# Kernel optimization log

Measured on AMD Instinct MI355X. Metric: run time of the kernel, lower is better.

Reference implementation:

```python
import jax, jax.numpy as jnp
import numpy as np

GROUPS = 32
EPS = 1e-5

def setup_inputs() -> dict:
    key = jax.random.key(0)
    ks = jax.random.split(key, 10)
    B, H, W, C = 2, 64, 64, 512
    s = 1.0 / np.sqrt(C)
    return {
        "x": jax.random.normal(ks[0], (B, H, W, C), dtype=jnp.float32),
        "gamma": jnp.ones((C,), jnp.float32),
        "beta": jnp.zeros((C,), jnp.float32),
        "wq": jax.random.normal(ks[1], (C, C), jnp.float32) * s,
        "bq": jnp.zeros((C,), jnp.float32),
        "wk": jax.random.normal(ks[2], (C, C), jnp.float32) * s,
        "bk": jnp.zeros((C,), jnp.float32),
        "wv": jax.random.normal(ks[3], (C, C), jnp.float32) * s,
        "bv": jnp.zeros((C,), jnp.float32),
        "wp": jax.random.normal(ks[4], (C, C), jnp.float32) * s,
        "bp": jnp.zeros((C,), jnp.float32),
    }

def _group_norm(x, gamma, beta):
    B, H, W, C = x.shape
    xg = x.reshape(B, H, W, GROUPS, C // GROUPS)
    mean = jnp.mean(xg, axis=(1, 2, 4), keepdims=True)
    var = jnp.var(xg, axis=(1, 2, 4), keepdims=True)
    xg = (xg - mean) * jax.lax.rsqrt(var + EPS)
    return xg.reshape(B, H, W, C) * gamma + beta

def reference(x, gamma, beta, wq, bq, wk, bk, wv, bv, wp, bp):
    B, H, W, C = x.shape
    h_ = _group_norm(x, gamma, beta)
    # 1x1 convs are per-pixel linear maps
    q = jnp.einsum("bhwc,cd->bhwd", h_, wq) + bq
    k = jnp.einsum("bhwc,cd->bhwd", h_, wk) + bk
    v = jnp.einsum("bhwc,cd->bhwd", h_, wv) + bv
    q = q.reshape(B, H * W, C)
    k = k.reshape(B, H * W, C)
    v = v.reshape(B, H * W, C)
    scale = C ** (-0.5)
    attn = jax.nn.softmax(jnp.einsum("bqc,bkc->bqk", q, k) * scale, axis=-1)
    out = jnp.einsum("bqk,bkc->bqc", attn, v).reshape(B, H, W, C)
    proj = jnp.einsum("bhwc,cd->bhwd", out, wp) + bp
    return x + proj
```

## Files before the change

kernel.cpp:

```cpp
#include <hip/hip_runtime.h>
#include <hip/hip_bf16.h>
#include <cstdint>
#include <cstddef>

typedef __bf16 bf16;
typedef bf16 bf16x8 __attribute__((ext_vector_type(8)));
typedef bf16 bf16x4 __attribute__((ext_vector_type(4)));
typedef float floatx4 __attribute__((ext_vector_type(4)));
typedef int intx8 __attribute__((ext_vector_type(8)));

#define DEVI __device__ __forceinline__

#define C_  512
#define HW_ 4096
#define B_  2
#define M_  8192
#define TK  64


DEVI floatx4 mfma16(bf16x8 a, bf16x8 b, floatx4 c) {
  return __builtin_amdgcn_mfma_f32_16x16x32_bf16(a, b, c, 0, 0, 0);
}

DEVI floatx4 mfma_fp8(intx8 a, intx8 b, floatx4 c) {
  return __builtin_amdgcn_mfma_scale_f32_16x16x128_f8f6f4(a, b, c, 0, 0,
                                                          0, 127, 0, 127);
}

DEVI void gload16(const void* g, void* lds) {
  using gp = const __attribute__((address_space(1))) unsigned int*;
  using lp = __attribute__((address_space(3))) unsigned int*;
  __builtin_amdgcn_global_load_lds(
      reinterpret_cast<gp>(reinterpret_cast<uintptr_t>(g)),
      reinterpret_cast<lp>((unsigned int)(uintptr_t)lds), 16, 0, 0);
}

DEVI uint32_t f32_to_fp8(float x) {
  return (uint32_t)__builtin_amdgcn_cvt_pk_fp8_f32(x, x, 0, false) & 0xffu;
}
DEVI int pack4_fp8(float a, float b, float c, float d) {
  int pk = __builtin_amdgcn_cvt_pk_fp8_f32(a, b, 0, false);
  return __builtin_amdgcn_cvt_pk_fp8_f32(c, d, pk, true);
}

__global__ __launch_bounds__(256) void gn_part(const float* __restrict__ x,
                                               float* __restrict__ pp,
                                               float* __restrict__ l) {
  int blk = blockIdx.x;
  int t = threadIdx.x;
  if (t < 16) l[blk * 16 + t] = 0.f;
  int batch = blk >> 8;
  int pix0 = (blk & 255) * 16;
  int c4 = (t & 127) << 2;
  int ph = t >> 7;
  const float* px = x + (size_t)batch * HW_ * C_ + (size_t)(pix0 + ph) * C_ + c4;
  float s1 = 0.f, s2 = 0.f;
#pragma unroll
  for (int i = 0; i < 8; i++) {
    float4 v = *reinterpret_cast<const float4*>(px + (size_t)i * 2 * C_);
    s1 += v.x + v.y + v.z + v.w;
    s2 += v.x * v.x + v.y * v.y + v.z * v.z + v.w * v.w;
  }
  __shared__ float l1[256], l2[256];
  l1[t] = s1; l2[t] = s2;
  __syncthreads();
  if (t < 32) {
    float a = 0.f, b2 = 0.f;
#pragma unroll
    for (int j = 0; j < 4; j++) {
      a  += l1[t * 4 + j] + l1[t * 4 + j + 128];
      b2 += l2[t * 4 + j] + l2[t * 4 + j + 128];
    }
    pp[blk * 32 + t] = a;
    pp[512 * 32 + blk * 32 + t] = b2;
  }
}

__global__ __launch_bounds__(256) void finish_wtrans(
    const float* __restrict__ pp, float* __restrict__ stats,
    const float* __restrict__ wq, const float* __restrict__ wk,
    const float* __restrict__ wv, const float* __restrict__ wp,
    uint8_t* __restrict__ w8, bf16* __restrict__ wtp) {
  int t = threadIdx.x;
  if (blockIdx.x < 64) {
    int bg = blockIdx.x;
    int b = bg >> 5, g = bg & 31;
    float s1 = pp[(b * 256 + t) * 32 + g];
    float s2 = pp[512 * 32 + (b * 256 + t) * 32 + g];
    for (int off = 32; off; off >>= 1) {
      s1 += __shfl_down(s1, off);
      s2 += __shfl_down(s2, off);
    }
    __shared__ float r1[4], r2[4];
    int wid = t >> 6;
    if ((t & 63) == 0) { r1[wid] = s1; r2[wid] = s2; }
    __syncthreads();
    if (t == 0) {
      s1 = r1[0] + r1[1] + r1[2] + r1[3];
      s2 = r2[0] + r2[1] + r2[2] + r2[3];
      float inv = 1.0f / (HW_ * 16);
      float mean = s1 * inv;
      float var  = s2 * inv - mean * mean;
      stats[bg]      = mean;
      stats[64 + bg] = rsqrtf(var + 1e-5f);
    }
    return;
  }
  int id = blockIdx.x - 64;
  int z = id >> 8;
  int k0 = ((id >> 4) & 15) * 32, n0 = (id & 15) * 32;
  const float* w = (z == 0) ? wq : (z == 1) ? wk : (z == 2) ? wv : wp;
  __shared__ float tt[32][33];
  int r = t >> 5, cc = t & 31;
  for (int i = 0; i < 4; i++) {
    int rr = r + i * 8;
    tt[rr][cc] = w[(size_t)(k0 + rr) * C_ + n0 + cc];
  }
  __syncthreads();
  if (z < 3) {
    uint8_t* dst = w8 + (size_t)z * C_ * C_;
    for (int i = 0; i < 4; i++) {
      int rr = r + i * 8;
      dst[(size_t)(n0 + rr) * C_ + k0 + cc] = (uint8_t)f32_to_fp8(tt[cc][rr]);
    }
  } else {
    for (int i = 0; i < 4; i++) {
      int rr = r + i * 8;
      wtp[(size_t)(n0 + rr) * C_ + k0 + cc] = (bf16)tt[cc][rr];
    }
  }
}

__global__ __launch_bounds__(256) void gn_apply(const float* __restrict__ x,
                                                const float* __restrict__ gamma,
                                                const float* __restrict__ beta,
                                                const float* __restrict__ stats,
                                                uint8_t* __restrict__ h8) {
  int idx = blockIdx.x * 256 + threadIdx.x;
  int m  = idx >> 7;
  int c4 = (idx & 127) << 2;
  int b = m >> 12;
  int g = c4 >> 4;
  float mean = stats[(b << 5) + g];
  float rs   = stats[64 + (b << 5) + g];
  const float4 xv = *reinterpret_cast<const float4*>(x + (size_t)m * C_ + c4);
  const float4 gv = *reinterpret_cast<const float4*>(gamma + c4);
  const float4 bv = *reinterpret_cast<const float4*>(beta + c4);
  int pk = pack4_fp8((xv.x - mean) * rs * gv.x + bv.x,
                     (xv.y - mean) * rs * gv.y + bv.y,
                     (xv.z - mean) * rs * gv.z + bv.z,
                     (xv.w - mean) * rs * gv.w + bv.w);
  *reinterpret_cast<int*>(h8 + (size_t)m * C_ + c4) = pk;
}

template <int BM, int BN, int MT, int NT>
DEVI void gemm_main(const bf16* __restrict__ A, int lda,
                    const bf16* __restrict__ Bt, int ldb,
                    int K, floatx4 (&acc)[MT][NT]) {
  constexpr int WCOLS = BN / (NT * 16);
  __shared__ __align__(16) bf16 As[BM * TK];
  __shared__ __align__(16) bf16 Bs[BN * TK];
  int tid = threadIdx.x;
  int w = tid >> 6, lane = tid & 63;
  int wrow = w / WCOLS, wcol = w % WCOLS;
  int col = lane & 15, quad = lane >> 4;
#pragma unroll
  for (int mt = 0; mt < MT; mt++)
#pragma unroll
    for (int nt = 0; nt < NT; nt++)
      acc[mt][nt] = floatx4{0.f, 0.f, 0.f, 0.f};
  for (int k0 = 0; k0 < K; k0 += TK) {
    __syncthreads();
#pragma unroll
    for (int i = 0; i < BM / 32; i++) {
      int id = tid + i * 256;
      gload16(A + (size_t)(id >> 3) * lda + k0 + (id & 7) * 8, As + id * 8);
    }
#pragma unroll
    for (int i = 0; i < BN / 32; i++) {
      int id = tid + i * 256;
      gload16(Bt + (size_t)(id >> 3) * ldb + k0 + (id & 7) * 8, Bs + id * 8);
    }
    __syncthreads();
#pragma unroll
    for (int kk = 0; kk < 2; kk++) {
      bf16x8 af[MT], bf[NT];
#pragma unroll
      for (int mt = 0; mt < MT; mt++)
        af[mt] = *reinterpret_cast<const bf16x8*>(
            As + (wrow * MT * 16 + mt * 16 + col) * TK + kk * 32 + quad * 8);
#pragma unroll
      for (int nt = 0; nt < NT; nt++)
        bf[nt] = *reinterpret_cast<const bf16x8*>(
            Bs + (wcol * NT * 16 + nt * 16 + col) * TK + kk * 32 + quad * 8);
#pragma unroll
      for (int mt = 0; mt < MT; mt++)
#pragma unroll
        for (int nt = 0; nt < NT; nt++)
          acc[mt][nt] = mfma16(af[mt], bf[nt], acc[mt][nt]);
    }
  }
}

template <int BM, int BN, int MT, int NT>
DEVI void gemm_fp8(const uint8_t* __restrict__ A, int lda,
                   const uint8_t* __restrict__ Bt, int ldb,
                   int K, floatx4 (&acc)[MT][NT]) {
  constexpr int WCOLS = BN / (NT * 16);
  __shared__ __align__(16) uint8_t As[BM * 128];
  __shared__ __align__(16) uint8_t Bs[BN * 128];
  int tid = threadIdx.x;
  int w = tid >> 6, lane = tid & 63;
  int wrow = w / WCOLS, wcol = w % WCOLS;
  int col = lane & 15, quad = lane >> 4;
#pragma unroll
  for (int mt = 0; mt < MT; mt++)
#pragma unroll
    for (int nt = 0; nt < NT; nt++)
      acc[mt][nt] = floatx4{0.f, 0.f, 0.f, 0.f};
  for (int k0 = 0; k0 < K; k0 += 128) {
    __syncthreads();
#pragma unroll
    for (int i = 0; i < BM / 32; i++) {
      int id = tid + i * 256;
      gload16(A + (size_t)(id >> 3) * lda + k0 + (id & 7) * 16, As + id * 16);
    }
#pragma unroll
    for (int i = 0; i < BN / 32; i++) {
      int id = tid + i * 256;
      gload16(Bt + (size_t)(id >> 3) * ldb + k0 + (id & 7) * 16, Bs + id * 16);
    }
    __syncthreads();
    intx8 af[MT], bf[NT];
#pragma unroll
    for (int mt = 0; mt < MT; mt++)
      af[mt] = *reinterpret_cast<const intx8*>(
          As + (wrow * MT * 16 + mt * 16 + col) * 128 + quad * 32);
#pragma unroll
    for (int nt = 0; nt < NT; nt++)
      bf[nt] = *reinterpret_cast<const intx8*>(
          Bs + (wcol * NT * 16 + nt * 16 + col) * 128 + quad * 32);
#pragma unroll
    for (int mt = 0; mt < MT; mt++)
#pragma unroll
      for (int nt = 0; nt < NT; nt++)
        acc[mt][nt] = mfma_fp8(af[mt], bf[nt], acc[mt][nt]);
  }
}

__global__ __launch_bounds__(256) void gemm_qkv(const uint8_t* __restrict__ h8,
                                                const uint8_t* __restrict__ w8,
                                                const float* __restrict__ bq,
                                                const float* __restrict__ bk,
                                                const float* __restrict__ bv,
                                                uint8_t* __restrict__ q8,
                                                uint8_t* __restrict__ k8,
                                                uint8_t* __restrict__ vt8) {
  int z = blockIdx.z;
  int m0 = blockIdx.x * 128, n0 = blockIdx.y * 64;
  floatx4 acc[2][4];
  gemm_fp8<128, 64, 2, 4>(h8 + (size_t)m0 * C_, C_,
                          w8 + (size_t)z * C_ * C_ + (size_t)n0 * C_, C_, C_, acc);
  int tid = threadIdx.x, w = tid >> 6, lane = tid & 63;
  int col = lane & 15, quad = lane >> 4;
  const float* bias = (z == 0) ? bq : (z == 1) ? bk : bv;
  if (z < 2) {
    uint8_t* out = (z == 0) ? q8 : k8;
#pragma unroll
    for (int mt = 0; mt < 2; mt++)
#pragma unroll
      for (int nt = 0; nt < 4; nt++) {
        int n = n0 + nt * 16 + col;
        float bb = bias[n];
#pragma unroll
        for (int r = 0; r < 4; r++) {
          int m = m0 + w * 32 + mt * 16 + quad * 4 + r;
          out[(size_t)m * C_ + n] = (uint8_t)f32_to_fp8(acc[mt][nt][r] + bb);
        }
      }
  } else {
#pragma unroll
    for (int mt = 0; mt < 2; mt++)
#pragma unroll
      for (int nt = 0; nt < 4; nt++) {
        int n = n0 + nt * 16 + col;
        float bb = bias[n];
        int mbase = m0 + w * 32 + mt * 16 + quad * 4;
        int b = mbase >> 12;
        int s = mbase & 4095;
        int pk = pack4_fp8(acc[mt][nt][0] + bb, acc[mt][nt][1] + bb,
                           acc[mt][nt][2] + bb, acc[mt][nt][3] + bb);
        *reinterpret_cast<int*>(vt8 + ((size_t)b * C_ + n) * HW_ + s) = pk;
      }
  }
}

__global__ __launch_bounds__(256) void gemm_qk(const uint8_t* __restrict__ q8,
                                               const uint8_t* __restrict__ k8,
                                               uint8_t* __restrict__ P8,
                                               float* __restrict__ l) {
  int b = blockIdx.z;
  int m0 = blockIdx.x * 128, n0 = blockIdx.y * 64;
  floatx4 acc[2][4];
  gemm_fp8<128, 64, 2, 4>(q8 + ((size_t)b * HW_ + m0) * C_, C_,
                          k8 + ((size_t)b * HW_ + n0) * C_, C_, C_, acc);
  int tid = threadIdx.x, w = tid >> 6, lane = tid & 63;
  int col = lane & 15, quad = lane >> 4;
  const float sl2e = 0.044194173824159216f * 1.4426950408889634f;
  uint8_t* Pb = P8 + (size_t)b * HW_ * HW_;
  float* lb = l + (size_t)b * HW_;
#pragma unroll
  for (int mt = 0; mt < 2; mt++) {
    float rs[4] = {0.f, 0.f, 0.f, 0.f};
#pragma unroll
    for (int nt = 0; nt < 4; nt++) {
      int n = n0 + nt * 16 + col;
      float p0 = exp2f(acc[mt][nt][0] * sl2e);
      float p1 = exp2f(acc[mt][nt][1] * sl2e);
      float p2 = exp2f(acc[mt][nt][2] * sl2e);
      float p3 = exp2f(acc[mt][nt][3] * sl2e);
      int pk = pack4_fp8(p0, p1, p2, p3);
      size_t base = (size_t)(m0 + w * 32 + mt * 16 + quad * 4) * HW_ + n;
      Pb[base]           = (uint8_t)pk;
      Pb[base + HW_]     = (uint8_t)((unsigned)pk >> 8);
      Pb[base + 2 * HW_] = (uint8_t)((unsigned)pk >> 16);
      Pb[base + 3 * HW_] = (uint8_t)((unsigned)pk >> 24);
      rs[0] += p0; rs[1] += p1; rs[2] += p2; rs[3] += p3;
    }
#pragma unroll
    for (int off = 1; off < 16; off <<= 1)
#pragma unroll
      for (int r = 0; r < 4; r++)
        rs[r] += __shfl_xor(rs[r], off);
    if (col == 0)
#pragma unroll
      for (int r = 0; r < 4; r++)
        atomicAdd(&lb[m0 + w * 32 + mt * 16 + quad * 4 + r], rs[r]);
  }
}

__global__ __launch_bounds__(256) void gemm_pv(const uint8_t* __restrict__ P8,
                                               const uint8_t* __restrict__ vt8,
                                               const float* __restrict__ l,
                                               bf16* __restrict__ o) {
  int b = blockIdx.z;
  int m0 = blockIdx.x * 128, n0 = blockIdx.y * 64;
  floatx4 acc[2][4];
  gemm_fp8<128, 64, 2, 4>(P8 + (size_t)b * HW_ * HW_ + (size_t)m0 * HW_, HW_,
                          vt8 + ((size_t)b * C_ + n0) * HW_, HW_, HW_, acc);
  int tid = threadIdx.x, w = tid >> 6, lane = tid & 63;
  int col = lane & 15, quad = lane >> 4;
  const float* lb = l + (size_t)b * HW_;
  bf16* ob = o + (size_t)b * HW_ * C_;
#pragma unroll
  for (int mt = 0; mt < 2; mt++)
#pragma unroll
    for (int r = 0; r < 4; r++) {
      int m = m0 + w * 32 + mt * 16 + quad * 4 + r;
      float inv = 1.0f / lb[m];
#pragma unroll
      for (int nt = 0; nt < 4; nt++) {
        int n = n0 + nt * 16 + col;
        ob[(size_t)m * C_ + n] = (bf16)(acc[mt][nt][r] * inv);
      }
    }
}

__global__ __launch_bounds__(256) void gemm_proj(const bf16* __restrict__ o,
                                                 const bf16* __restrict__ wtp,
                                                 const float* __restrict__ bp,
                                                 const float* __restrict__ x,
                                                 float* __restrict__ out) {
  int m0 = blockIdx.x * 128, n0 = blockIdx.y * 64;
  floatx4 acc[2][4];
  gemm_main<128, 64, 2, 4>(o + (size_t)m0 * C_, C_, wtp + (size_t)n0 * C_, C_, C_, acc);
  int tid = threadIdx.x, w = tid >> 6, lane = tid & 63;
  int col = lane & 15, quad = lane >> 4;
#pragma unroll
  for (int mt = 0; mt < 2; mt++)
#pragma unroll
    for (int nt = 0; nt < 4; nt++) {
      int n = n0 + nt * 16 + col;
      float bb = bp[n];
#pragma unroll
      for (int r = 0; r < 4; r++) {
        int m = m0 + w * 32 + mt * 16 + quad * 4 + r;
        out[(size_t)m * C_ + n] = x[(size_t)m * C_ + n] + acc[mt][nt][r] + bb;
      }
    }
}

extern "C" void kernel_launch(void* const* d_in, const int* in_sizes, int n_in,
                              void* d_out, int out_size, void* d_ws, size_t ws_size,
                              hipStream_t stream) {
  const float* x     = (const float*)d_in[0];
  const float* gamma = (const float*)d_in[1];
  const float* beta  = (const float*)d_in[2];
  const float* wq    = (const float*)d_in[3];
  const float* bq    = (const float*)d_in[4];
  const float* wk    = (const float*)d_in[5];
  const float* bk    = (const float*)d_in[6];
  const float* wv    = (const float*)d_in[7];
  const float* bv    = (const float*)d_in[8];
  const float* wp    = (const float*)d_in[9];
  const float* bp    = (const float*)d_in[10];
  float* out = (float*)d_out;

  char* w8s = (char*)d_ws;
  float* stats = (float*)(w8s);
  float* l     = (float*)(w8s + 65536u);
  float* pp    = (float*)(w8s + 393216u);
  uint8_t* w8  = (uint8_t*)(w8s + (1u << 20));
  bf16* wtp    = (bf16*)(w8s + (2u << 20));
  uint8_t* h8  = (uint8_t*)(w8s + (4u << 20));
  bf16* o      = (bf16*)(w8s + (8u << 20));
  uint8_t* q8  = (uint8_t*)(w8s + (16u << 20));
  uint8_t* k8  = (uint8_t*)(w8s + (20u << 20));
  uint8_t* vt8 = (uint8_t*)(w8s + (24u << 20));
  uint8_t* P8  = (uint8_t*)(w8s + (28u << 20));

  gn_part<<<512, 256, 0, stream>>>(x, pp, l);
  finish_wtrans<<<1088, 256, 0, stream>>>(pp, stats, wq, wk, wv, wp, w8, wtp);
  gn_apply<<<4096, 256, 0, stream>>>(x, gamma, beta, stats, h8);
  gemm_qkv<<<dim3(M_ / 128, C_ / 64, 3), 256, 0, stream>>>(h8, w8, bq, bk, bv, q8, k8, vt8);
  gemm_qk<<<dim3(HW_ / 128, HW_ / 64, B_), 256, 0, stream>>>(q8, k8, P8, l);
  gemm_pv<<<dim3(HW_ / 128, C_ / 64, B_), 256, 0, stream>>>(P8, vt8, l, o);
  gemm_proj<<<dim3(M_ / 128, C_ / 64, 1), 256, 0, stream>>>(o, wtp, bp, x, out);
}
```

Before: 194.0 us.

## Double-buffer LDS tiles in bf16 and fp8 GEMM mainloops

Both GEMM helpers now keep two LDS buffers and issue the global-to-LDS loads for the next K tile before computing on the current one. This cuts one barrier per iteration and lets the memory loads overlap the MFMA work. In exchange, LDS use per block doubles, which may lower occupancy. The hand-written waitcnt and barrier sequence has to stay correct for the async loads.

```diff
diff --git a/kernel.cpp b/kernel.cpp
--- a/kernel.cpp
+++ b/kernel.cpp
@@ -158,8 +158,8 @@
                     const bf16* __restrict__ Bt, int ldb,
                     int K, floatx4 (&acc)[MT][NT]) {
   constexpr int WCOLS = BN / (NT * 16);
-  __shared__ __align__(16) bf16 As[BM * TK];
-  __shared__ __align__(16) bf16 Bs[BN * TK];
+  __shared__ __align__(16) bf16 As[2][BM * TK];
+  __shared__ __align__(16) bf16 Bs[2][BN * TK];
   int tid = threadIdx.x;
   int w = tid >> 6, lane = tid & 63;
   int wrow = w / WCOLS, wcol = w % WCOLS;
@@ -169,35 +169,48 @@
 #pragma unroll
     for (int nt = 0; nt < NT; nt++)
       acc[mt][nt] = floatx4{0.f, 0.f, 0.f, 0.f};
-  for (int k0 = 0; k0 < K; k0 += TK) {
-    __syncthreads();
+
+  auto stage = [&](int k0, bf16* as, bf16* bs) {
 #pragma unroll
     for (int i = 0; i < BM / 32; i++) {
       int id = tid + i * 256;
-      gload16(A + (size_t)(id >> 3) * lda + k0 + (id & 7) * 8, As + id * 8);
+      gload16(A + (size_t)(id >> 3) * lda + k0 + (id & 7) * 8, as + id * 8);
     }
 #pragma unroll
     for (int i = 0; i < BN / 32; i++) {
       int id = tid + i * 256;
-      gload16(Bt + (size_t)(id >> 3) * ldb + k0 + (id & 7) * 8, Bs + id * 8);
-    }
-    __syncthreads();
+      gload16(Bt + (size_t)(id >> 3) * ldb + k0 + (id & 7) * 8, bs + id * 8);
+    }
+  };
+
+  stage(0, As[0], Bs[0]);
+  asm volatile("s_waitcnt vmcnt(0)" ::: "memory");
+  __builtin_amdgcn_s_barrier();
+  const int nIter = K / TK;
+  int cur = 0;
+  for (int t = 0; t < nIter; t++) {
+    if (t + 1 < nIter) stage((t + 1) * TK, As[cur ^ 1], Bs[cur ^ 1]);
 #pragma unroll
     for (int kk = 0; kk < 2; kk++) {
-      bf16x8 af[MT], bf[NT];
+      bf16x8 af[MT], bfr[NT];
 #pragma unroll
       for (int mt = 0; mt < MT; mt++)
         af[mt] = *reinterpret_cast<const bf16x8*>(
-            As + (wrow * MT * 16 + mt * 16 + col) * TK + kk * 32 + quad * 8);
+            As[cur] + (wrow * MT * 16 + mt * 16 + col) * TK + kk * 32 + quad * 8);
 #pragma unroll
       for (int nt = 0; nt < NT; nt++)
-        bf[nt] = *reinterpret_cast<const bf16x8*>(
-            Bs + (wcol * NT * 16 + nt * 16 + col) * TK + kk * 32 + quad * 8);
+        bfr[nt] = *reinterpret_cast<const bf16x8*>(
+            Bs[cur] + (wcol * NT * 16 + nt * 16 + col) * TK + kk * 32 + quad * 8);
 #pragma unroll
       for (int mt = 0; mt < MT; mt++)
 #pragma unroll
         for (int nt = 0; nt < NT; nt++)
-          acc[mt][nt] = mfma16(af[mt], bf[nt], acc[mt][nt]);
+          acc[mt][nt] = mfma16(af[mt], bfr[nt], acc[mt][nt]);
+    }
+    if (t + 1 < nIter) {
+      asm volatile("s_waitcnt vmcnt(0) lgkmcnt(0)" ::: "memory");
+      __builtin_amdgcn_s_barrier();
+      cur ^= 1;
     }
   }
 }
@@ -207,8 +220,8 @@
                    const uint8_t* __restrict__ Bt, int ldb,
                    int K, floatx4 (&acc)[MT][NT]) {
   constexpr int WCOLS = BN / (NT * 16);
-  __shared__ __align__(16) uint8_t As[BM * 128];
-  __shared__ __align__(16) uint8_t Bs[BN * 128];
+  __shared__ __align__(16) uint8_t As[2][BM * 128];
+  __shared__ __align__(16) uint8_t Bs[2][BN * 128];
   int tid = threadIdx.x;
   int w = tid >> 6, lane = tid & 63;
   int wrow = w / WCOLS, wcol = w % WCOLS;
@@ -218,33 +231,46 @@
 #pragma unroll
     for (int nt = 0; nt < NT; nt++)
       acc[mt][nt] = floatx4{0.f, 0.f, 0.f, 0.f};
-  for (int k0 = 0; k0 < K; k0 += 128) {
-    __syncthreads();
+
+  auto stage = [&](int k0, uint8_t* as, uint8_t* bs) {
 #pragma unroll
     for (int i = 0; i < BM / 32; i++) {
       int id = tid + i * 256;
-      gload16(A + (size_t)(id >> 3) * lda + k0 + (id & 7) * 16, As + id * 16);
+      gload16(A + (size_t)(id >> 3) * lda + k0 + (id & 7) * 16, as + id * 16);
     }
 #pragma unroll
     for (int i = 0; i < BN / 32; i++) {
       int id = tid + i * 256;
-      gload16(Bt + (size_t)(id >> 3) * ldb + k0 + (id & 7) * 16, Bs + id * 16);
-    }
-    __syncthreads();
-    intx8 af[MT], bf[NT];
+      gload16(Bt + (size_t)(id >> 3) * ldb + k0 + (id & 7) * 16, bs + id * 16);
+    }
+  };
+
+  stage(0, As[0], Bs[0]);
+  asm volatile("s_waitcnt vmcnt(0)" ::: "memory");
+  __builtin_amdgcn_s_barrier();
+  const int nIter = K >> 7;
+  int cur = 0;
+  for (int t = 0; t < nIter; t++) {
+    if (t + 1 < nIter) stage((t + 1) << 7, As[cur ^ 1], Bs[cur ^ 1]);
+    intx8 af[MT], bfr[NT];
 #pragma unroll
     for (int mt = 0; mt < MT; mt++)
       af[mt] = *reinterpret_cast<const intx8*>(
-          As + (wrow * MT * 16 + mt * 16 + col) * 128 + quad * 32);
+          As[cur] + (wrow * MT * 16 + mt * 16 + col) * 128 + quad * 32);
 #pragma unroll
     for (int nt = 0; nt < NT; nt++)
-      bf[nt] = *reinterpret_cast<const intx8*>(
-          Bs + (wcol * NT * 16 + nt * 16 + col) * 128 + quad * 32);
+      bfr[nt] = *reinterpret_cast<const intx8*>(
+          Bs[cur] + (wcol * NT * 16 + nt * 16 + col) * 128 + quad * 32);
 #pragma unroll
     for (int mt = 0; mt < MT; mt++)
 #pragma unroll
       for (int nt = 0; nt < NT; nt++)
-        acc[mt][nt] = mfma_fp8(af[mt], bf[nt], acc[mt][nt]);
+        acc[mt][nt] = mfma_fp8(af[mt], bfr[nt], acc[mt][nt]);
+    if (t + 1 < nIter) {
+      asm volatile("s_waitcnt vmcnt(0) lgkmcnt(0)" ::: "memory");
+      __builtin_amdgcn_s_barrier();
+      cur ^= 1;
+    }
   }
 }
 
```

Result: slower. 199.8 us (+3.0%).
